# Optimization experiments

Hardware: AMD Instinct MI355X
Metric: run time of the kernel (lower is better)

Reference implementation:

```python
import jax, jax.numpy as jnp
import numpy as np

B, NQ, NK = 16, 2048, 2048
KD, QD, KQ = 256, 256, 256
CLIP = 10.0


def setup_inputs() -> dict:
    key = jax.random.key(0)
    k1, k2, k3, k4, k5 = jax.random.split(key, 5)
    k_inputs = jax.random.normal(k1, (B, NK, KD), dtype=jnp.float32)
    q_inputs = jax.random.normal(k2, (B, NQ, QD), dtype=jnp.float32)
    adjancy = jax.random.randint(k3, (B, NQ, NK), 0, 2, dtype=jnp.int32)
    # Linear init in source: (rand - 0.5) * 0.05 -> uniform(-0.025, 0.025)
    Wk = jax.random.uniform(k4, (KD, KQ), dtype=jnp.float32, minval=-0.025, maxval=0.025)
    Wq = jax.random.uniform(k5, (QD, KQ), dtype=jnp.float32, minval=-0.025, maxval=0.025)
    return {"k_inputs": k_inputs, "q_inputs": q_inputs, "adjancy": adjancy, "Wk": Wk, "Wq": Wq}


def reference(k_inputs, q_inputs, adjancy, Wk, Wq):
    k = jnp.einsum("bnd,de->bne", k_inputs, Wk)          # [B, NK, KQ]
    q = jnp.einsum("bmd,de->bme", q_inputs, Wq)          # [B, NQ, KQ]
    scale = 1.0 / jnp.sqrt(jnp.asarray(KQ, dtype=q.dtype))
    scores = jnp.einsum("bme,bne->bmn", q, k) * scale     # [B, NQ, NK]
    scores = jnp.tanh(scores) * CLIP                      # clip is not None
    scores = jnp.where(adjancy.astype(bool), scores, -jnp.inf)
    return jax.nn.softmax(scores, axis=2)
```

## Files before the change

kernel.cpp:

```cpp
#include <hip/hip_runtime.h>

#define BATCH 16
#define NQ 2048
#define NK 2048

typedef short s16x8 __attribute__((ext_vector_type(8)));
typedef __bf16 bf16x8 __attribute__((ext_vector_type(8)));
typedef float f32x16 __attribute__((ext_vector_type(16)));
typedef float f32x4 __attribute__((ext_vector_type(4)));
typedef int i32x4 __attribute__((ext_vector_type(4)));
typedef unsigned u32x2 __attribute__((ext_vector_type(2)));

static __device__ __forceinline__ unsigned short f2bf(float f) {
  unsigned u = __builtin_bit_cast(unsigned, f);
  u += 0x7FFFu + ((u >> 16) & 1u);
  return (unsigned short)(u >> 16);
}

static __device__ __forceinline__ f32x16 mfma32(s16x8 a, s16x8 b, f32x16 c) {
  return __builtin_amdgcn_mfma_f32_32x32x16_bf16(
      __builtin_bit_cast(bf16x8, a), __builtin_bit_cast(bf16x8, b), c, 0, 0, 0);
}

static __device__ __forceinline__ f32x4 mfma16(s16x8 a, s16x8 b, f32x4 c) {
  return __builtin_amdgcn_mfma_f32_16x16x32_bf16(
      __builtin_bit_cast(bf16x8, a), __builtin_bit_cast(bf16x8, b), c, 0, 0, 0);
}

static __device__ __forceinline__ float score_p(float s) {
  float u = __builtin_amdgcn_exp2f(s * 2.885390081777927f);
  return __builtin_amdgcn_exp2f(-28.853900817779268f * __builtin_amdgcn_rcpf(u + 1.0f));
}

__global__ void prep_wt(const float* __restrict__ Wk, unsigned short* __restrict__ WkT,
                        const float* __restrict__ Wq, unsigned short* __restrict__ WqT) {
  const float* W = blockIdx.y ? Wq : Wk;
  unsigned short* WT = blockIdx.y ? WqT : WkT;
  float scale = blockIdx.y ? 0.0625f : 1.0f;
  int idx = blockIdx.x * 256 + threadIdx.x;
  int n = idx >> 8, k = idx & 255;
  WT[n * 256 + k] = f2bf(W[k * 256 + n] * scale);
}

__global__ __launch_bounds__(256, 2) void proj_kernel(
    const float* __restrict__ Xk, const unsigned short* __restrict__ WkT,
    unsigned short* __restrict__ Yk,
    const float* __restrict__ Xq, const unsigned short* __restrict__ WqT,
    unsigned short* __restrict__ Yq) {
  const float* X;
  const unsigned short* WT;
  unsigned short* Y;
  if (blockIdx.y == 0) { X = Xk; WT = WkT; Y = Yk; }
  else                 { X = Xq; WT = WqT; Y = Yq; }

  int tid = threadIdx.x;
  int wave = tid >> 6, lane = tid & 63;
  int l31 = lane & 31, kh = lane >> 5;
  int r0 = blockIdx.x * 128 + wave * 32;

  const float* xp = X + (size_t)(r0 + l31) * 256 + kh * 8;

  f32x16 acc[8];
#pragma unroll
  for (int ct = 0; ct < 8; ++ct)
#pragma unroll
    for (int i = 0; i < 16; ++i) acc[ct][i] = 0.0f;

#pragma unroll
  for (int kk = 0; kk < 16; ++kk) {
    f32x4 a0 = *(const f32x4*)(xp + kk * 16);
    f32x4 a1 = *(const f32x4*)(xp + kk * 16 + 4);
    s16x8 af;
#pragma unroll
    for (int j = 0; j < 4; ++j) {
      af[j]     = (short)f2bf(a0[j]);
      af[4 + j] = (short)f2bf(a1[j]);
    }
#pragma unroll
    for (int ct = 0; ct < 8; ++ct) {
      s16x8 bw = *(const s16x8*)(WT + (size_t)(ct * 32 + l31) * 256 + kk * 16 + kh * 8);
      acc[ct] = mfma32(af, bw, acc[ct]);
    }
  }

  int kg2 = l31 >> 3, j = l31 & 7;
#pragma unroll
  for (int ct = 0; ct < 8; ++ct) {
#pragma unroll
    for (int r = 0; r < 16; ++r) {
      int rrow = (r & 3) + 8 * (r >> 2) + 4 * kh;
      int row = r0 + rrow;
      Y[((size_t)((row >> 4) * 8 + ct) * 64 + kg2 * 16 + (row & 15)) * 8 + j] =
          f2bf(acc[ct][r]);
    }
  }
}

__global__ __launch_bounds__(512, 1) void attn_kernel(
    const unsigned short* __restrict__ Kf, const unsigned short* __restrict__ Qf,
    const int* __restrict__ adj, float* __restrict__ out) {
  int lin = blockIdx.y * 64 + blockIdx.x;
  int b  = (lin & 7) * 2 + ((lin >> 3) & 1);
  int qt = lin >> 4;
  int q0 = qt * 32;
  int tid = threadIdx.x;
  int wave = tid >> 6, lane = tid & 63;
  int l15 = lane & 15, kg = lane >> 4;
  int colbase = wave * 256;

  __shared__ unsigned plds[8 * 16 * 256];
  __shared__ unsigned lmask[8 * 288];
  __shared__ float wsum[8][32];
  __shared__ float rrecip[32];

  const i32x4* ap4 =
      (const i32x4*)(adj + ((size_t)b * NQ + q0) * (size_t)NK + colbase) + lane;
  unsigned* lm = lmask + wave * 288;
#pragma unroll
  for (int chunk = 0; chunk < 2; ++chunk) {
    i32x4 av[16];
#pragma unroll
    for (int r = 0; r < 16; ++r)
      av[r] = __builtin_nontemporal_load(ap4 + (size_t)(chunk * 16 + r) * (NK / 4));
#pragma unroll
    for (int r = 0; r < 16; ++r) {
      i32x4 v = av[r];
      unsigned nib = (v[0] != 0 ? 1u : 0u) | (v[1] != 0 ? 2u : 0u) |
                     (v[2] != 0 ? 4u : 0u) | (v[3] != 0 ? 8u : 0u);
      unsigned m = nib << ((lane & 7) * 4);
      m |= __shfl_xor(m, 1);
      m |= __shfl_xor(m, 2);
      m |= __shfl_xor(m, 4);
      if ((lane & 7) == 0) lm[(chunk * 16 + r) * 9 + (lane >> 3)] = m;
    }
  }

  const unsigned short* qpA = Qf + (size_t)(b * 128 + 2 * qt) * 4096;
  s16x8 aqA[8], aqB[8];
#pragma unroll
  for (int kk = 0; kk < 8; ++kk) {
    aqA[kk] = __builtin_nontemporal_load(
        (const s16x8*)(qpA + ((size_t)kk * 64 + lane) * 8));
    aqB[kk] = __builtin_nontemporal_load(
        (const s16x8*)(qpA + 4096 + ((size_t)kk * 64 + lane) * 8));
  }


  const unsigned short* kfb = Kf + (size_t)b * 128 * 4096;
  unsigned* pl = plds + wave * 4096 + lane * 2;

  float rsumA[4] = {0.0f, 0.0f, 0.0f, 0.0f};
  float rsumB[4] = {0.0f, 0.0f, 0.0f, 0.0f};
  s16x8 bkX[8], bkY[8];

#define KLOAD(CT, DST)                                                         \
  {                                                                            \
    const unsigned short* kpt = kfb + (size_t)(wave * 16 + (CT)) * 4096;       \
    _Pragma("unroll") for (int kk = 0; kk < 8; ++kk)                           \
        DST[kk] = *(const s16x8*)(kpt + ((size_t)kk * 64 + lane) * 8);         \
  }

#define PROCESS(CT, BK)                                                        \
  {                                                                            \
    f32x4 accA = {0.0f, 0.0f, 0.0f, 0.0f};                                     \
    f32x4 accB = {0.0f, 0.0f, 0.0f, 0.0f};                                     \
    _Pragma("unroll") for (int kk = 0; kk < 8; ++kk) {                         \
      accA = mfma16(aqA[kk], BK[kk], accA);                                    \
      accB = mfma16(aqB[kk], BK[kk], accB);                                    \
    }                                                                          \
    unsigned shift = (unsigned)(((CT) & 1) * 16 + l15);                        \
    float pA[4], pB[4];                                                        \
    _Pragma("unroll") for (int r = 0; r < 4; ++r) {                            \
      unsigned mwA = lm[(kg * 4 + r) * 9 + ((CT) >> 1)];                       \
      unsigned mwB = lm[(16 + kg * 4 + r) * 9 + ((CT) >> 1)];                  \
      float eA = score_p(accA[r]);                                             \
      float eB = score_p(accB[r]);                                             \
      pA[r] = ((mwA >> shift) & 1u) ? eA : 0.0f;                               \
      pB[r] = ((mwB >> shift) & 1u) ? eB : 0.0f;                               \
      rsumA[r] += pA[r];                                                       \
      rsumB[r] += pB[r];                                                       \
    }                                                                          \
    u32x2 vA, vB;                                                              \
    vA[0] = (unsigned)f2bf(pA[0]) | ((unsigned)f2bf(pA[1]) << 16);             \
    vA[1] = (unsigned)f2bf(pA[2]) | ((unsigned)f2bf(pA[3]) << 16);             \
    vB[0] = (unsigned)f2bf(pB[0]) | ((unsigned)f2bf(pB[1]) << 16);             \
    vB[1] = (unsigned)f2bf(pB[2]) | ((unsigned)f2bf(pB[3]) << 16);             \
    *(u32x2*)(pl + (CT)*256) = vA;                                             \
    *(u32x2*)(pl + (CT)*256 + 128) = vB;                                       \
  }

  KLOAD(0, bkX)
#pragma unroll
  for (int cp = 0; cp < 8; ++cp) {
    KLOAD(2 * cp + 1, bkY)
    PROCESS(2 * cp, bkX)
    if (cp < 7) KLOAD(2 * cp + 2, bkX)
    PROCESS(2 * cp + 1, bkY)
  }
#undef KLOAD
#undef PROCESS

#pragma unroll
  for (int r = 0; r < 4; ++r) {
    float vA = rsumA[r], vB = rsumB[r];
    vA += __shfl_xor(vA, 1);  vB += __shfl_xor(vB, 1);
    vA += __shfl_xor(vA, 2);  vB += __shfl_xor(vB, 2);
    vA += __shfl_xor(vA, 4);  vB += __shfl_xor(vB, 4);
    vA += __shfl_xor(vA, 8);  vB += __shfl_xor(vB, 8);
    rsumA[r] = vA;  rsumB[r] = vB;
  }
  if (l15 == 0) {
#pragma unroll
    for (int r = 0; r < 4; ++r) {
      wsum[wave][kg * 4 + r]      = rsumA[r];
      wsum[wave][16 + kg * 4 + r] = rsumB[r];
    }
  }
  __syncthreads();
  if (tid < 32) {
    float s = 0.0f;
#pragma unroll
    for (int w = 0; w < 8; ++w) s += wsum[w][tid];
    rrecip[tid] = 1.0f / s;
  }
  __syncthreads();

  float rcA[4], rcB[4];
#pragma unroll
  for (int r = 0; r < 4; ++r) {
    rcA[r] = rrecip[kg * 4 + r];
    rcB[r] = rrecip[16 + kg * 4 + r];
  }

  float* opA = out + ((size_t)b * NQ + q0 + kg * 4) * (size_t)NK + colbase + l15;
  float* opB = opA + (size_t)16 * NK;
#pragma unroll 4
  for (int ct = 0; ct < 16; ++ct) {
    u32x2 vA = *(const u32x2*)(pl + ct * 256);
    u32x2 vB = *(const u32x2*)(pl + ct * 256 + 128);
#pragma unroll
    for (int r = 0; r < 4; ++r) {
      unsigned w = (r < 2) ? vA[0] : vA[1];
      float p = __builtin_bit_cast(float, (r & 1) ? (w & 0xffff0000u) : (w << 16));
      __builtin_nontemporal_store(p * rcA[r], opA + (size_t)r * NK + ct * 16);
    }
#pragma unroll
    for (int r = 0; r < 4; ++r) {
      unsigned w = (r < 2) ? vB[0] : vB[1];
      float p = __builtin_bit_cast(float, (r & 1) ? (w & 0xffff0000u) : (w << 16));
      __builtin_nontemporal_store(p * rcB[r], opB + (size_t)r * NK + ct * 16);
    }
  }
}

extern "C" void kernel_launch(void* const* d_in, const int* in_sizes, int n_in,
                              void* d_out, int out_size, void* d_ws, size_t ws_size,
                              hipStream_t stream) {
  const float* k_in = (const float*)d_in[0];
  const float* q_in = (const float*)d_in[1];
  const int* adj    = (const int*)d_in[2];
  const float* Wk   = (const float*)d_in[3];
  const float* Wq   = (const float*)d_in[4];
  float* out = (float*)d_out;

  char* ws = (char*)d_ws;
  unsigned short* WkT = (unsigned short*)(ws);
  unsigned short* WqT = (unsigned short*)(ws + (1u << 17));
  unsigned short* Kf  = (unsigned short*)(ws + (1u << 18));
  unsigned short* Qf  = (unsigned short*)(ws + (1u << 18) + (1u << 24));

  prep_wt<<<dim3(256, 2), 256, 0, stream>>>(Wk, WkT, Wq, WqT);

  proj_kernel<<<dim3(256, 2), 256, 0, stream>>>(k_in, WkT, Kf, q_in, WqT, Qf);

  attn_kernel<<<dim3(64, 16), 512, 0, stream>>>(Kf, Qf, adj, out);
}
```

Before: 238.9 us.

## Make attention blocks persistent over four query tiles with prefetch overlap

The attention grid shrinks from 1024 to 256 blocks, and each block now loops over four consecutive 32-row query tiles of one batch. While one tile's normalized probabilities are being stored, the next tile's adjacency mask, Q fragments and first K tile are loaded. This aims to hide load latency behind the output writes and to cut per-block startup cost. The trade-off is fewer resident blocks for the scheduler to balance and a serialized per-block loop.

```diff
diff --git a/kernel.cpp b/kernel.cpp
--- a/kernel.cpp
+++ b/kernel.cpp
@@ -99,10 +99,9 @@
 __global__ __launch_bounds__(512, 1) void attn_kernel(
     const unsigned short* __restrict__ Kf, const unsigned short* __restrict__ Qf,
     const int* __restrict__ adj, float* __restrict__ out) {
-  int lin = blockIdx.y * 64 + blockIdx.x;
+  int lin = blockIdx.y * 16 + blockIdx.x;
   int b  = (lin & 7) * 2 + ((lin >> 3) & 1);
-  int qt = lin >> 4;
-  int q0 = qt * 32;
+  int tb = lin >> 4;
   int tid = threadIdx.x;
   int wave = tid >> 6, lane = tid & 63;
   int l15 = lane & 15, kg = lane >> 4;
@@ -113,45 +112,41 @@
   __shared__ float wsum[8][32];
   __shared__ float rrecip[32];
 
+  const unsigned short* kfb = Kf + (size_t)b * 128 * 4096;
+  unsigned* pl = plds + wave * 4096 + lane * 2;
+  unsigned* lm = lmask + wave * 288;
+
+  int q0 = tb * 128;
   const i32x4* ap4 =
       (const i32x4*)(adj + ((size_t)b * NQ + q0) * (size_t)NK + colbase) + lane;
-  unsigned* lm = lmask + wave * 288;
-#pragma unroll
-  for (int chunk = 0; chunk < 2; ++chunk) {
-    i32x4 av[16];
-#pragma unroll
-    for (int r = 0; r < 16; ++r)
-      av[r] = __builtin_nontemporal_load(ap4 + (size_t)(chunk * 16 + r) * (NK / 4));
-#pragma unroll
-    for (int r = 0; r < 16; ++r) {
-      i32x4 v = av[r];
-      unsigned nib = (v[0] != 0 ? 1u : 0u) | (v[1] != 0 ? 2u : 0u) |
-                     (v[2] != 0 ? 4u : 0u) | (v[3] != 0 ? 8u : 0u);
-      unsigned m = nib << ((lane & 7) * 4);
-      m |= __shfl_xor(m, 1);
-      m |= __shfl_xor(m, 2);
-      m |= __shfl_xor(m, 4);
-      if ((lane & 7) == 0) lm[(chunk * 16 + r) * 9 + (lane >> 3)] = m;
-    }
-  }
-
-  const unsigned short* qpA = Qf + (size_t)(b * 128 + 2 * qt) * 4096;
-  s16x8 aqA[8], aqB[8];
-#pragma unroll
-  for (int kk = 0; kk < 8; ++kk) {
-    aqA[kk] = __builtin_nontemporal_load(
-        (const s16x8*)(qpA + ((size_t)kk * 64 + lane) * 8));
-    aqB[kk] = __builtin_nontemporal_load(
-        (const s16x8*)(qpA + 4096 + ((size_t)kk * 64 + lane) * 8));
-  }
-
-
-  const unsigned short* kfb = Kf + (size_t)b * 128 * 4096;
-  unsigned* pl = plds + wave * 4096 + lane * 2;
-
-  float rsumA[4] = {0.0f, 0.0f, 0.0f, 0.0f};
-  float rsumB[4] = {0.0f, 0.0f, 0.0f, 0.0f};
-  s16x8 bkX[8], bkY[8];
+  const unsigned short* qp = Qf + (size_t)(b * 128 + tb * 8) * 4096;
+  float* opBase = out + ((size_t)b * NQ + q0 + kg * 4) * (size_t)NK + colbase + l15;
+
+  s16x8 aqA[8], aqB[8], bkX[8], bkY[8];
+
+#define ADJ_LOAD(BASE, AV)                                                     \
+  _Pragma("unroll") for (int r = 0; r < 16; ++r)                               \
+      AV[r] = __builtin_nontemporal_load(ap4 + (size_t)((BASE) + r) * (NK / 4));
+
+#define ADJ_PACK(BASE, AV)                                                     \
+  _Pragma("unroll") for (int r = 0; r < 16; ++r) {                             \
+    i32x4 v = AV[r];                                                           \
+    unsigned nib = (v[0] != 0 ? 1u : 0u) | (v[1] != 0 ? 2u : 0u) |             \
+                   (v[2] != 0 ? 4u : 0u) | (v[3] != 0 ? 8u : 0u);              \
+    unsigned m = nib << ((lane & 7) * 4);                                      \
+    m |= __shfl_xor(m, 1);                                                     \
+    m |= __shfl_xor(m, 2);                                                     \
+    m |= __shfl_xor(m, 4);                                                     \
+    if ((lane & 7) == 0) lm[((BASE) + r) * 9 + (lane >> 3)] = m;               \
+  }
+
+#define QLOAD                                                                  \
+  _Pragma("unroll") for (int kk = 0; kk < 8; ++kk) {                           \
+    aqA[kk] = __builtin_nontemporal_load(                                      \
+        (const s16x8*)(qp + ((size_t)kk * 64 + lane) * 8));                    \
+    aqB[kk] = __builtin_nontemporal_load(                                      \
+        (const s16x8*)(qp + 4096 + ((size_t)kk * 64 + lane) * 8));             \
+  }
 
 #define KLOAD(CT, DST)                                                         \
   {                                                                            \
@@ -189,68 +184,107 @@
     *(u32x2*)(pl + (CT)*256 + 128) = vB;                                       \
   }
 
+#define STORE_CT(CT, OPA, OPB)                                                 \
+  {                                                                            \
+    u32x2 vA = *(const u32x2*)(pl + (CT)*256);                                 \
+    u32x2 vB = *(const u32x2*)(pl + (CT)*256 + 128);                           \
+    _Pragma("unroll") for (int r = 0; r < 4; ++r) {                            \
+      unsigned w = (r < 2) ? vA[0] : vA[1];                                    \
+      float p = __builtin_bit_cast(float, (r & 1) ? (w & 0xffff0000u) : (w << 16)); \
+      __builtin_nontemporal_store(p * rcA[r], OPA + (size_t)r * NK + (CT)*16); \
+    }                                                                          \
+    _Pragma("unroll") for (int r = 0; r < 4; ++r) {                            \
+      unsigned w = (r < 2) ? vB[0] : vB[1];                                    \
+      float p = __builtin_bit_cast(float, (r & 1) ? (w & 0xffff0000u) : (w << 16)); \
+      __builtin_nontemporal_store(p * rcB[r], OPB + (size_t)r * NK + (CT)*16); \
+    }                                                                          \
+  }
+
+  {
+    i32x4 av[16];
+    ADJ_LOAD(0, av)
+    ADJ_PACK(0, av)
+    ADJ_LOAD(16, av)
+    ADJ_PACK(16, av)
+  }
+  QLOAD
   KLOAD(0, bkX)
-#pragma unroll
-  for (int cp = 0; cp < 8; ++cp) {
-    KLOAD(2 * cp + 1, bkY)
-    PROCESS(2 * cp, bkX)
-    if (cp < 7) KLOAD(2 * cp + 2, bkX)
-    PROCESS(2 * cp + 1, bkY)
-  }
+
+#pragma unroll 1
+  for (int t = 0; t < 4; ++t) {
+    float rsumA[4] = {0.0f, 0.0f, 0.0f, 0.0f};
+    float rsumB[4] = {0.0f, 0.0f, 0.0f, 0.0f};
+
+#pragma unroll
+    for (int cp = 0; cp < 8; ++cp) {
+      KLOAD(2 * cp + 1, bkY)
+      PROCESS(2 * cp, bkX)
+      if (cp < 7) KLOAD(2 * cp + 2, bkX)
+      PROCESS(2 * cp + 1, bkY)
+    }
+
+#pragma unroll
+    for (int r = 0; r < 4; ++r) {
+      float vA = rsumA[r], vB = rsumB[r];
+      vA += __shfl_xor(vA, 1);  vB += __shfl_xor(vB, 1);
+      vA += __shfl_xor(vA, 2);  vB += __shfl_xor(vB, 2);
+      vA += __shfl_xor(vA, 4);  vB += __shfl_xor(vB, 4);
+      vA += __shfl_xor(vA, 8);  vB += __shfl_xor(vB, 8);
+      rsumA[r] = vA;  rsumB[r] = vB;
+    }
+    if (l15 == 0) {
+#pragma unroll
+      for (int r = 0; r < 4; ++r) {
+        wsum[wave][kg * 4 + r]      = rsumA[r];
+        wsum[wave][16 + kg * 4 + r] = rsumB[r];
+      }
+    }
+    __syncthreads();
+    if (tid < 32) {
+      float s = 0.0f;
+#pragma unroll
+      for (int w = 0; w < 8; ++w) s += wsum[w][tid];
+      rrecip[tid] = 1.0f / s;
+    }
+    __syncthreads();
+
+    float rcA[4], rcB[4];
+#pragma unroll
+    for (int r = 0; r < 4; ++r) {
+      rcA[r] = rrecip[kg * 4 + r];
+      rcB[r] = rrecip[16 + kg * 4 + r];
+    }
+
+    float* opA = opBase;
+    float* opB = opBase + (size_t)16 * NK;
+    bool more = (t < 3);
+
+    ap4 += (size_t)32 * (NK / 4);
+    qp  += 8192;
+    opBase += (size_t)32 * NK;
+
+    i32x4 av[16];
+    if (more) { ADJ_LOAD(0, av) }
+#pragma unroll
+    for (int ct = 0; ct < 8; ++ct) { STORE_CT(ct, opA, opB) }
+    if (more) {
+      ADJ_PACK(0, av)
+      ADJ_LOAD(16, av)
+    }
+#pragma unroll
+    for (int ct = 8; ct < 16; ++ct) { STORE_CT(ct, opA, opB) }
+    if (more) {
+      ADJ_PACK(16, av)
+      QLOAD
+      KLOAD(0, bkX)
+    }
+  }
+#undef ADJ_LOAD
+#undef ADJ_PACK
+#undef QLOAD
 #undef KLOAD
 #undef PROCESS
-
-#pragma unroll
-  for (int r = 0; r < 4; ++r) {
-    float vA = rsumA[r], vB = rsumB[r];
-    vA += __shfl_xor(vA, 1);  vB += __shfl_xor(vB, 1);
-    vA += __shfl_xor(vA, 2);  vB += __shfl_xor(vB, 2);
-    vA += __shfl_xor(vA, 4);  vB += __shfl_xor(vB, 4);
-    vA += __shfl_xor(vA, 8);  vB += __shfl_xor(vB, 8);
-    rsumA[r] = vA;  rsumB[r] = vB;
-  }
-  if (l15 == 0) {
-#pragma unroll
-    for (int r = 0; r < 4; ++r) {
-      wsum[wave][kg * 4 + r]      = rsumA[r];
-      wsum[wave][16 + kg * 4 + r] = rsumB[r];
-    }
-  }
-  __syncthreads();
-  if (tid < 32) {
-    float s = 0.0f;
-#pragma unroll
-    for (int w = 0; w < 8; ++w) s += wsum[w][tid];
-    rrecip[tid] = 1.0f / s;
-  }
-  __syncthreads();
-
-  float rcA[4], rcB[4];
-#pragma unroll
-  for (int r = 0; r < 4; ++r) {
-    rcA[r] = rrecip[kg * 4 + r];
-    rcB[r] = rrecip[16 + kg * 4 + r];
-  }
-
-  float* opA = out + ((size_t)b * NQ + q0 + kg * 4) * (size_t)NK + colbase + l15;
-  float* opB = opA + (size_t)16 * NK;
-#pragma unroll 4
-  for (int ct = 0; ct < 16; ++ct) {
-    u32x2 vA = *(const u32x2*)(pl + ct * 256);
-    u32x2 vB = *(const u32x2*)(pl + ct * 256 + 128);
-#pragma unroll
-    for (int r = 0; r < 4; ++r) {
-      unsigned w = (r < 2) ? vA[0] : vA[1];
-      float p = __builtin_bit_cast(float, (r & 1) ? (w & 0xffff0000u) : (w << 16));
-      __builtin_nontemporal_store(p * rcA[r], opA + (size_t)r * NK + ct * 16);
-    }
-#pragma unroll
-    for (int r = 0; r < 4; ++r) {
-      unsigned w = (r < 2) ? vB[0] : vB[1];
-      float p = __builtin_bit_cast(float, (r & 1) ? (w & 0xffff0000u) : (w << 16));
-      __builtin_nontemporal_store(p * rcB[r], opB + (size_t)r * NK + ct * 16);
-    }
-  }
+#undef STORE_CT
 }
 
 extern "C" void kernel_launch(void* const* d_in, const int* in_sizes, int n_in,
@@ -273,5 +307,5 @@
 
   proj_kernel<<<dim3(256, 2), 256, 0, stream>>>(k_in, WkT, Kf, q_in, WqT, Qf);
 
-  attn_kernel<<<dim3(64, 16), 512, 0, stream>>>(Kf, Qf, adj, out);
-}
+  attn_kernel<<<dim3(16, 16), 512, 0, stream>>>(Kf, Qf, adj, out);
+}
```

Result: slower. 550.4 us (+130.4%).

## Pack adjacency into bitmask in separate kernel before attention

Applied to the files above, without the earlier changes.

Adds a pack_adj kernel that reads the int32 adjacency matrix once and compresses it into a per-row bitmask with wave ballots. The attention kernel then loads only 256 bytes of mask per row instead of converting the int32 data inline, and needs a block barrier after staging the mask in shared memory. Output stores switch from nontemporal to normal stores. The full adjacency read now happens in its own launch, so it no longer overlaps with attention compute, and the mask adds an extra global write and read.

```diff
diff --git a/kernel.cpp b/kernel.cpp
--- a/kernel.cpp
+++ b/kernel.cpp
@@ -40,6 +40,21 @@
   int idx = blockIdx.x * 256 + threadIdx.x;
   int n = idx >> 8, k = idx & 255;
   WT[n * 256 + k] = f2bf(W[k * 256 + n] * scale);
+}
+
+__global__ __launch_bounds__(256) void pack_adj(const int* __restrict__ adj,
+                                                unsigned* __restrict__ mask) {
+  int gwave = (blockIdx.x * 256 + threadIdx.x) >> 6;
+  int lane = threadIdx.x & 63;
+  const int* p = adj + (size_t)gwave * 2048;
+  unsigned my = 0;
+#pragma unroll
+  for (int c = 0; c < 32; ++c) {
+    int a = p[c * 64 + lane];
+    unsigned long long m = __ballot(a != 0);
+    if ((lane >> 1) == c) my = (lane & 1) ? (unsigned)(m >> 32) : (unsigned)m;
+  }
+  mask[(size_t)gwave * 64 + lane] = my;
 }
 
 __global__ __launch_bounds__(256, 2) void proj_kernel(
@@ -98,7 +113,7 @@
 
 __global__ __launch_bounds__(512, 1) void attn_kernel(
     const unsigned short* __restrict__ Kf, const unsigned short* __restrict__ Qf,
-    const int* __restrict__ adj, float* __restrict__ out) {
+    const unsigned* __restrict__ mask, float* __restrict__ out) {
   int lin = blockIdx.y * 64 + blockIdx.x;
   int b  = (lin & 7) * 2 + ((lin >> 3) & 1);
   int qt = lin >> 4;
@@ -109,30 +124,15 @@
   int colbase = wave * 256;
 
   __shared__ unsigned plds[8 * 16 * 256];
-  __shared__ unsigned lmask[8 * 288];
+  __shared__ unsigned lmask[32 * 68];
   __shared__ float wsum[8][32];
   __shared__ float rrecip[32];
 
-  const i32x4* ap4 =
-      (const i32x4*)(adj + ((size_t)b * NQ + q0) * (size_t)NK + colbase) + lane;
-  unsigned* lm = lmask + wave * 288;
-#pragma unroll
-  for (int chunk = 0; chunk < 2; ++chunk) {
-    i32x4 av[16];
-#pragma unroll
-    for (int r = 0; r < 16; ++r)
-      av[r] = __builtin_nontemporal_load(ap4 + (size_t)(chunk * 16 + r) * (NK / 4));
-#pragma unroll
-    for (int r = 0; r < 16; ++r) {
-      i32x4 v = av[r];
-      unsigned nib = (v[0] != 0 ? 1u : 0u) | (v[1] != 0 ? 2u : 0u) |
-                     (v[2] != 0 ? 4u : 0u) | (v[3] != 0 ? 8u : 0u);
-      unsigned m = nib << ((lane & 7) * 4);
-      m |= __shfl_xor(m, 1);
-      m |= __shfl_xor(m, 2);
-      m |= __shfl_xor(m, 4);
-      if ((lane & 7) == 0) lm[(chunk * 16 + r) * 9 + (lane >> 3)] = m;
-    }
+  {
+    const i32x4* msrc = (const i32x4*)(mask + ((size_t)b * NQ + q0) * 64);
+    i32x4 v = msrc[tid];
+    int row = tid >> 4, w4 = tid & 15;
+    *(i32x4*)(lmask + row * 68 + w4 * 4) = v;
   }
 
   const unsigned short* qpA = Qf + (size_t)(b * 128 + 2 * qt) * 4096;
@@ -145,6 +145,7 @@
         (const s16x8*)(qpA + 4096 + ((size_t)kk * 64 + lane) * 8));
   }
 
+  __syncthreads();
 
   const unsigned short* kfb = Kf + (size_t)b * 128 * 4096;
   unsigned* pl = plds + wave * 4096 + lane * 2;
@@ -169,10 +170,11 @@
       accB = mfma16(aqB[kk], BK[kk], accB);                                    \
     }                                                                          \
     unsigned shift = (unsigned)(((CT) & 1) * 16 + l15);                        \
+    int wrd = wave * 8 + ((CT) >> 1);                                          \
     float pA[4], pB[4];                                                        \
     _Pragma("unroll") for (int r = 0; r < 4; ++r) {                            \
-      unsigned mwA = lm[(kg * 4 + r) * 9 + ((CT) >> 1)];                       \
-      unsigned mwB = lm[(16 + kg * 4 + r) * 9 + ((CT) >> 1)];                  \
+      unsigned mwA = lmask[(kg * 4 + r) * 68 + wrd];                           \
+      unsigned mwB = lmask[(16 + kg * 4 + r) * 68 + wrd];                      \
       float eA = score_p(accA[r]);                                             \
       float eB = score_p(accB[r]);                                             \
       pA[r] = ((mwA >> shift) & 1u) ? eA : 0.0f;                               \
@@ -242,13 +244,13 @@
     for (int r = 0; r < 4; ++r) {
       unsigned w = (r < 2) ? vA[0] : vA[1];
       float p = __builtin_bit_cast(float, (r & 1) ? (w & 0xffff0000u) : (w << 16));
-      __builtin_nontemporal_store(p * rcA[r], opA + (size_t)r * NK + ct * 16);
+      opA[(size_t)r * NK + ct * 16] = p * rcA[r];
     }
 #pragma unroll
     for (int r = 0; r < 4; ++r) {
       unsigned w = (r < 2) ? vB[0] : vB[1];
       float p = __builtin_bit_cast(float, (r & 1) ? (w & 0xffff0000u) : (w << 16));
-      __builtin_nontemporal_store(p * rcB[r], opB + (size_t)r * NK + ct * 16);
+      opB[(size_t)r * NK + ct * 16] = p * rcB[r];
     }
   }
 }
@@ -268,10 +270,13 @@
   unsigned short* WqT = (unsigned short*)(ws + (1u << 17));
   unsigned short* Kf  = (unsigned short*)(ws + (1u << 18));
   unsigned short* Qf  = (unsigned short*)(ws + (1u << 18) + (1u << 24));
+  unsigned* maskbuf   = (unsigned*)(ws + (1u << 18) + (2u << 24));
 
   prep_wt<<<dim3(256, 2), 256, 0, stream>>>(Wk, WkT, Wq, WqT);
 
+  pack_adj<<<(BATCH * NQ * NK) / (2048 * 4), 256, 0, stream>>>(adj, maskbuf);
+
   proj_kernel<<<dim3(256, 2), 256, 0, stream>>>(k_in, WkT, Kf, q_in, WqT, Qf);
 
-  attn_kernel<<<dim3(64, 16), 512, 0, stream>>>(Kf, Qf, adj, out);
-}
+  attn_kernel<<<dim3(64, 16), 512, 0, stream>>>(Kf, Qf, maskbuf, out);
+}
```

Measured after the change: 251.3 us. 5.2% more time.
